# Kernel optimization log

Hardware: AMD Instinct MI355X
Metric: run time of the kernel (lower is better)

## Reference

```python
import jax, jax.numpy as jnp
import numpy as np
from jax import lax

M_RANGE = 1  # padding = m_range, kernel is (2*m_range+1)^2 = 9 classes of 3x3


def _conv(x, kernel):
    # torch F.conv2d (cross-correlation), stride 1, padding M_RANGE
    return lax.conv_general_dilated(
        x, kernel, window_strides=(1, 1),
        padding=[(M_RANGE, M_RANGE), (M_RANGE, M_RANGE)],
        dimension_numbers=('NCHW', 'OIHW', 'NCHW'))


def _construct_seg(ones, m_mask, m_kernel):
    # ones.expand_as(m_mask) * m_mask, then per-sample conv2d -> batched conv
    return _conv(ones * m_mask, m_kernel)  # [B,1,H,W]


def _construct_image(im, m_mask, appear, m_kernel):
    # im: [B,C,H,W]; m_mask: [B,K,H,W]; appear: [B,1,H,W]
    im = im * appear
    B, C, H, W = im.shape
    K = m_mask.shape[1]
    # fuse the python double loop: fold (B,C) into batch, conv K->1 once
    im_expand = (im[:, :, None, :, :] * m_mask[:, None, :, :, :]).reshape(B * C, K, H, W)
    return _conv(im_expand, m_kernel).reshape(B, C, H, W)


def setup_inputs() -> dict:
    key = jax.random.key(0)
    k0, k1, k2, k3 = jax.random.split(key, 4)
    B, C, H, W, K, N_INPUTS = 32, 3, 256, 256, 9, 2
    im_input_f = jax.random.uniform(k0, (B, N_INPUTS * C, H, W), dtype=jnp.float32)
    im_input_b = jax.random.uniform(k1, (B, N_INPUTS * C, H, W), dtype=jnp.float32)
    ones = jnp.ones((B, 1, H, W), dtype=jnp.float32)
    # gt motion masks: soft per-pixel distribution over K motion classes
    gt_motion_f = jax.nn.softmax(jax.random.normal(k2, (B, K, H, W), dtype=jnp.float32), axis=1)
    gt_motion_b = jax.nn.softmax(jax.random.normal(k3, (B, K, H, W), dtype=jnp.float32), axis=1)
    # one-hot displacement kernels: kernel i has a 1 at flat position i of the 3x3 window
    m_kernel = jnp.eye(K, dtype=jnp.float32).reshape(K, 3, 3)[None]  # [1,K,3,3]
    return {"im_input_f": im_input_f, "im_input_b": im_input_b, "ones": ones,
            "gt_motion_f": gt_motion_f, "gt_motion_b": gt_motion_b, "m_kernel": m_kernel}


def reference(im_input_f, im_input_b, ones, gt_motion_f, gt_motion_b, m_kernel):
    IM_CHANNEL = 3
    relu = jax.nn.relu
    m_mask_f, m_mask_b = gt_motion_f, gt_motion_b

    seg_f = _construct_seg(ones, m_mask_f, m_kernel)
    seg_b = _construct_seg(ones, m_mask_b, m_kernel)

    disappear_f = relu(seg_f - 1)
    appear_f = relu(1 - disappear_f)
    disappear_b = relu(seg_b - 1)
    appear_b = relu(1 - disappear_b)

    pred_f = _construct_image(im_input_f[:, -IM_CHANNEL:, :, :], m_mask_f, appear_f, m_kernel)
    pred_b = _construct_image(im_input_b[:, -IM_CHANNEL:, :, :], m_mask_b, appear_b, m_kernel)

    seg_f = 1 - relu(1 - seg_f)
    seg_b = 1 - relu(1 - seg_b)
    attn = (seg_f + 1e-5) / (seg_f + seg_b + 2e-5)  # [B,1,H,W], broadcasts over C
    pred = attn * pred_f + (1 - attn) * pred_b
    return (pred, m_mask_f, 1 - appear_f, attn, m_mask_b, 1 - appear_b, 1 - attn)
```

## Files before the change

kernel.cpp:

```cpp
#include <hip/hip_runtime.h>

#define BB 32
#define KK 9
#define CC 3
#define HH 256
#define WW 256
#define HW (HH * WW)

#define SZ_P ((size_t)BB * CC * HW)
#define SZ_M ((size_t)BB * KK * HW)
#define SZ_S ((size_t)BB * HW)

#define TX 64
#define TY 16
#define TILES_X (WW / TX)
#define TILES_Y (HH / TY)
#define TILES_PER_B (TILES_X * TILES_Y)

__global__ __launch_bounds__(256) void fused_binet_kernel(
    const float* __restrict__ im_f, const float* __restrict__ im_b,
    const float* __restrict__ gt_f, const float* __restrict__ gt_b,
    float* __restrict__ out) {
  __shared__ float s_sf[TY + 2][TX + 2];
  __shared__ float s_sb[TY + 2][TX + 2];

  int bid = blockIdx.x;
  int b = bid / TILES_PER_B;
  int t = bid % TILES_PER_B;
  int ty0 = (t / TILES_X) * TY;
  int tx0 = (t % TILES_X) * TX;

  const float* gf  = gt_f + (size_t)b * KK * HW;
  const float* gb  = gt_b + (size_t)b * KK * HW;
  const float* imf = im_f + ((size_t)b * 6 + 3) * HW;
  const float* imb = im_b + ((size_t)b * 6 + 3) * HW;

  int tid = threadIdx.x;

  for (int i = tid; i < (TY + 2) * (TX + 2); i += 256) {
    int ly = i / (TX + 2);
    int lx = i - ly * (TX + 2);
    int y = ty0 + ly - 1;
    int x = tx0 + lx - 1;
    float sf = 0.f, sb = 0.f;
    if (y >= 0 && y < HH && x >= 0 && x < WW) {
#pragma unroll
      for (int k = 0; k < KK; ++k) {
        int yy = y + (k / 3) - 1;
        int xx = x + (k % 3) - 1;
        if (yy >= 0 && yy < HH && xx >= 0 && xx < WW) {
          int off = k * HW + (yy << 8) + xx;
          sf += gf[off];
          sb += gb[off];
        }
      }
    }
    s_sf[ly][lx] = sf;
    s_sb[ly][lx] = sb;
  }
  __syncthreads();

  float* o_mf     = out + SZ_P;
  float* o_disf   = out + SZ_P + SZ_M;
  float* o_attn   = o_disf + SZ_S;
  float* o_mb     = o_attn + SZ_S;
  float* o_disb   = o_mb + SZ_M;
  float* o_1mattn = o_disb + SZ_S;

  int lx  = tid & (TX - 1);
  int ly0 = tid >> 6;

#pragma unroll
  for (int r = 0; r < 4; ++r) {
    int ly = ly0 + r * 4;
    int h = ty0 + ly;
    int w = tx0 + lx;
    int hw = (h << 8) + w;
    size_t sidx = (size_t)b * HW + hw;

    float sf = s_sf[ly + 1][lx + 1];
    float sb = s_sb[ly + 1][lx + 1];
    float dis_f = fmaxf(sf - 1.f, 0.f);
    float app_f = fmaxf(1.f - dis_f, 0.f);
    float dis_b = fmaxf(sb - 1.f, 0.f);
    float app_b = fmaxf(1.f - dis_b, 0.f);
    float sfc = 1.f - fmaxf(1.f - sf, 0.f);
    float sbc = 1.f - fmaxf(1.f - sb, 0.f);
    float attn = (sfc + 1e-5f) / (sfc + sbc + 2e-5f);

    o_disf[sidx]   = 1.f - app_f;
    o_attn[sidx]   = attn;
    o_disb[sidx]   = 1.f - app_b;
    o_1mattn[sidx] = 1.f - attn;

    float pf0 = 0.f, pf1 = 0.f, pf2 = 0.f;
    float pb0 = 0.f, pb1 = 0.f, pb2 = 0.f;
#pragma unroll
    for (int k = 0; k < KK; ++k) {
      size_t moff = (size_t)b * KK * HW + (size_t)k * HW + hw;
      o_mf[moff] = gf[k * HW + hw];
      o_mb[moff] = gb[k * HW + hw];

      int y = h + (k / 3) - 1;
      int x = w + (k % 3) - 1;
      if (y >= 0 && y < HH && x >= 0 && x < WW) {
        int p = (y << 8) + x;
        float sfq = s_sf[ly + (k / 3)][lx + (k % 3)];
        float af = fmaxf(1.f - fmaxf(sfq - 1.f, 0.f), 0.f);
        float cf = af * gf[k * HW + p];
        pf0 = fmaf(cf, imf[p], pf0);
        pf1 = fmaf(cf, imf[HW + p], pf1);
        pf2 = fmaf(cf, imf[2 * HW + p], pf2);
        float sbq = s_sb[ly + (k / 3)][lx + (k % 3)];
        float ab = fmaxf(1.f - fmaxf(sbq - 1.f, 0.f), 0.f);
        float cb = ab * gb[k * HW + p];
        pb0 = fmaf(cb, imb[p], pb0);
        pb1 = fmaf(cb, imb[HW + p], pb1);
        pb2 = fmaf(cb, imb[2 * HW + p], pb2);
      }
    }
    float at2 = 1.f - attn;
    size_t pbase = (size_t)b * CC * HW + hw;
    out[pbase]          = fmaf(attn, pf0, at2 * pb0);
    out[pbase + HW]     = fmaf(attn, pf1, at2 * pb1);
    out[pbase + 2 * HW] = fmaf(attn, pf2, at2 * pb2);
  }
}

extern "C" void kernel_launch(void* const* d_in, const int* in_sizes, int n_in,
                              void* d_out, int out_size, void* d_ws, size_t ws_size,
                              hipStream_t stream) {
  const float* im_f = (const float*)d_in[0];
  const float* im_b = (const float*)d_in[1];
  const float* gt_f = (const float*)d_in[3];
  const float* gt_b = (const float*)d_in[4];
  float* out = (float*)d_out;

  dim3 block(256);
  dim3 grid(BB * TILES_PER_B);

  fused_binet_kernel<<<grid, block, 0, stream>>>(im_f, im_b, gt_f, gt_b, out);
}
```

Before: 458.0 us.

## Rewrite fused kernel with full-row tiles, float4 vectors, shuffles and nontemporal stores

Each block now covers full 256-wide rows, 8 rows per block, with one wavefront per row and each lane owning 4 consecutive pixels. Horizontal neighbours come from wavefront shuffles instead of redundant global reads. The forward and backward passes run one after the other through a shared 10-row seg buffer. Mask copies and outputs use float4 nontemporal stores, and block IDs are swizzled. This is meant to cut the redundant scalar global loads of the old tiled version and raise memory efficiency, at the cost of higher register pressure from holding nine float4 mask rows per pass.

```diff
diff --git a/kernel.cpp b/kernel.cpp
--- a/kernel.cpp
+++ b/kernel.cpp
@@ -11,120 +11,171 @@
 #define SZ_M ((size_t)BB * KK * HW)
 #define SZ_S ((size_t)BB * HW)
 
-#define TX 64
-#define TY 16
-#define TILES_X (WW / TX)
-#define TILES_Y (HH / TY)
-#define TILES_PER_B (TILES_X * TILES_Y)
+typedef float f4 __attribute__((ext_vector_type(4)));
 
-__global__ __launch_bounds__(256) void fused_binet_kernel(
+__device__ __forceinline__ f4 ld4(const float* p) { return *(const f4*)p; }
+__device__ __forceinline__ void ntst4(float* p, f4 v) {
+  __builtin_nontemporal_store(v, (f4*)p);
+}
+__device__ __forceinline__ f4 vmax4(f4 a, f4 b) {
+  return __builtin_elementwise_max(a, b);
+}
+__device__ __forceinline__ f4 app4(f4 s) {
+  f4 one = {1.f, 1.f, 1.f, 1.f}, z = {0.f, 0.f, 0.f, 0.f};
+  return vmax4(one - vmax4(s - one, z), z);
+}
+__device__ __forceinline__ float app1(float s) {
+  return fmaxf(1.f - fmaxf(s - 1.f, 0.f), 0.f);
+}
+__device__ __forceinline__ f4 shiftwin(f4 v, int dx, int lane) {
+  if (dx == 0) {
+    float l = __shfl_up(v.w, 1);
+    if (lane == 0) l = 0.f;
+    return (f4){l, v.x, v.y, v.z};
+  } else if (dx == 2) {
+    float r = __shfl_down(v.x, 1);
+    if (lane == 63) r = 0.f;
+    return (f4){v.y, v.z, v.w, r};
+  }
+  return v;
+}
+
+__device__ __forceinline__ void run_pass(
+    const float* __restrict__ g,
+    const float* __restrict__ im,
+    float* __restrict__ o_m,
+    float (*s_seg)[WW],
+    int w, int lane, int x0, int y0, int y, size_t hw,
+    f4& seg_out, f4& p0, f4& p1, f4& p2) {
+  const f4 z = {0.f, 0.f, 0.f, 0.f};
+  f4 r[KK];
+  f4 seg = z;
+#pragma unroll
+  for (int k = 0; k < KK; ++k) {
+    const int dy = k / 3, dx = k % 3;
+    int yr = y + dy - 1;
+    f4 v = z;
+    if ((unsigned)yr < HH)
+      v = ld4(g + (size_t)k * HW + ((size_t)yr << 8) + x0);
+    f4 wv = shiftwin(v, dx, lane);
+    r[k] = wv;
+    seg += wv;
+    f4 c = (dy == 1) ? v : ld4(g + (size_t)k * HW + hw);
+    ntst4(o_m + (size_t)k * HW + hw, c);
+  }
+  *(f4*)&s_seg[w + 1][x0] = seg;
+
+  if (w < 2) {
+    int lr = (w == 0) ? 0 : 9;
+    int yh = (w == 0) ? y0 - 1 : y0 + 8;
+    f4 s = z;
+#pragma unroll
+    for (int k = 0; k < KK; ++k) {
+      const int dy = k / 3, dx = k % 3;
+      int yr = yh + dy - 1;
+      f4 v = z;
+      if ((unsigned)yr < HH)
+        v = ld4(g + (size_t)k * HW + ((size_t)yr << 8) + x0);
+      s += shiftwin(v, dx, lane);
+    }
+    *(f4*)&s_seg[lr][x0] = s;
+  }
+  __syncthreads();
+
+  p0 = z; p1 = z; p2 = z;
+#pragma unroll
+  for (int dy = 0; dy < 3; ++dy) {
+    const float* srow = s_seg[w + dy];
+    f4 sc = *(const f4*)&srow[x0];
+    float sl = srow[(x0 == 0) ? 0 : (x0 - 1)];
+    float sr = srow[(x0 == WW - 4) ? (WW - 1) : (x0 + 4)];
+    f4 ac = app4(sc);
+    float al = app1(sl), ar = app1(sr);
+
+    int yr = y + dy - 1;
+    f4 i0 = z, i1 = z, i2 = z;
+    if ((unsigned)yr < HH) {
+      size_t rb = ((size_t)yr << 8) + x0;
+      i0 = ld4(im + rb);
+      i1 = ld4(im + HW + rb);
+      i2 = ld4(im + 2 * HW + rb);
+    }
+    float i0l = __shfl_up(i0.w, 1), i0r = __shfl_down(i0.x, 1);
+    float i1l = __shfl_up(i1.w, 1), i1r = __shfl_down(i1.x, 1);
+    float i2l = __shfl_up(i2.w, 1), i2r = __shfl_down(i2.x, 1);
+#pragma unroll
+    for (int dx = 0; dx < 3; ++dx) {
+      const int k = 3 * dy + dx;
+      f4 aw = (dx == 0) ? (f4){al, ac.x, ac.y, ac.z}
+            : (dx == 2) ? (f4){ac.y, ac.z, ac.w, ar} : ac;
+      f4 c = aw * r[k];
+      f4 w0 = (dx == 0) ? (f4){i0l, i0.x, i0.y, i0.z}
+            : (dx == 2) ? (f4){i0.y, i0.z, i0.w, i0r} : i0;
+      f4 w1 = (dx == 0) ? (f4){i1l, i1.x, i1.y, i1.z}
+            : (dx == 2) ? (f4){i1.y, i1.z, i1.w, i1r} : i1;
+      f4 w2 = (dx == 0) ? (f4){i2l, i2.x, i2.y, i2.z}
+            : (dx == 2) ? (f4){i2.y, i2.z, i2.w, i2r} : i2;
+      p0 += c * w0;
+      p1 += c * w1;
+      p2 += c * w2;
+    }
+  }
+  __syncthreads();
+  seg_out = seg;
+}
+
+__global__ __launch_bounds__(512) void fused_binet_kernel(
     const float* __restrict__ im_f, const float* __restrict__ im_b,
     const float* __restrict__ gt_f, const float* __restrict__ gt_b,
     float* __restrict__ out) {
-  __shared__ float s_sf[TY + 2][TX + 2];
-  __shared__ float s_sb[TY + 2][TX + 2];
+  __shared__ float s_seg[10][WW];
 
   int bid = blockIdx.x;
-  int b = bid / TILES_PER_B;
-  int t = bid % TILES_PER_B;
-  int ty0 = (t / TILES_X) * TY;
-  int tx0 = (t % TILES_X) * TX;
+  int actual = ((bid & 7) << 7) | (bid >> 3);
+  int b  = actual >> 5;
+  int y0 = (actual & 31) << 3;
+
+  int tid  = threadIdx.x;
+  int w    = tid >> 6;
+  int lane = tid & 63;
+  int x0   = lane << 2;
+  int y    = y0 + w;
+  size_t hw = ((size_t)y << 8) + x0;
 
   const float* gf  = gt_f + (size_t)b * KK * HW;
   const float* gb  = gt_b + (size_t)b * KK * HW;
   const float* imf = im_f + ((size_t)b * 6 + 3) * HW;
   const float* imb = im_b + ((size_t)b * 6 + 3) * HW;
 
-  int tid = threadIdx.x;
-
-  for (int i = tid; i < (TY + 2) * (TX + 2); i += 256) {
-    int ly = i / (TX + 2);
-    int lx = i - ly * (TX + 2);
-    int y = ty0 + ly - 1;
-    int x = tx0 + lx - 1;
-    float sf = 0.f, sb = 0.f;
-    if (y >= 0 && y < HH && x >= 0 && x < WW) {
-#pragma unroll
-      for (int k = 0; k < KK; ++k) {
-        int yy = y + (k / 3) - 1;
-        int xx = x + (k % 3) - 1;
-        if (yy >= 0 && yy < HH && xx >= 0 && xx < WW) {
-          int off = k * HW + (yy << 8) + xx;
-          sf += gf[off];
-          sb += gb[off];
-        }
-      }
-    }
-    s_sf[ly][lx] = sf;
-    s_sb[ly][lx] = sb;
-  }
-  __syncthreads();
-
-  float* o_mf     = out + SZ_P;
+  float* o_mf     = out + SZ_P + (size_t)b * KK * HW;
   float* o_disf   = out + SZ_P + SZ_M;
   float* o_attn   = o_disf + SZ_S;
-  float* o_mb     = o_attn + SZ_S;
-  float* o_disb   = o_mb + SZ_M;
+  float* o_mb     = o_attn + SZ_S + (size_t)b * KK * HW;
+  float* o_disb   = o_attn + SZ_S + SZ_M;
   float* o_1mattn = o_disb + SZ_S;
 
-  int lx  = tid & (TX - 1);
-  int ly0 = tid >> 6;
+  f4 segf, segb, pf0, pf1, pf2, pb0, pb1, pb2;
+  run_pass(gf, imf, o_mf, s_seg, w, lane, x0, y0, y, hw, segf, pf0, pf1, pf2);
+  run_pass(gb, imb, o_mb, s_seg, w, lane, x0, y0, y, hw, segb, pb0, pb1, pb2);
 
-#pragma unroll
-  for (int r = 0; r < 4; ++r) {
-    int ly = ly0 + r * 4;
-    int h = ty0 + ly;
-    int w = tx0 + lx;
-    int hw = (h << 8) + w;
-    size_t sidx = (size_t)b * HW + hw;
+  f4 one = {1.f, 1.f, 1.f, 1.f}, z = {0.f, 0.f, 0.f, 0.f};
+  f4 appf = app4(segf);
+  f4 appb = app4(segb);
+  f4 sfc = one - vmax4(one - segf, z);
+  f4 sbc = one - vmax4(one - segb, z);
+  f4 attn = (sfc + 1e-5f) / (sfc + sbc + 2e-5f);
+  f4 at2 = one - attn;
 
-    float sf = s_sf[ly + 1][lx + 1];
-    float sb = s_sb[ly + 1][lx + 1];
-    float dis_f = fmaxf(sf - 1.f, 0.f);
-    float app_f = fmaxf(1.f - dis_f, 0.f);
-    float dis_b = fmaxf(sb - 1.f, 0.f);
-    float app_b = fmaxf(1.f - dis_b, 0.f);
-    float sfc = 1.f - fmaxf(1.f - sf, 0.f);
-    float sbc = 1.f - fmaxf(1.f - sb, 0.f);
-    float attn = (sfc + 1e-5f) / (sfc + sbc + 2e-5f);
+  size_t sidx = (size_t)b * HW + hw;
+  ntst4(o_disf + sidx, one - appf);
+  ntst4(o_attn + sidx, attn);
+  ntst4(o_disb + sidx, one - appb);
+  ntst4(o_1mattn + sidx, one - attn);
 
-    o_disf[sidx]   = 1.f - app_f;
-    o_attn[sidx]   = attn;
-    o_disb[sidx]   = 1.f - app_b;
-    o_1mattn[sidx] = 1.f - attn;
-
-    float pf0 = 0.f, pf1 = 0.f, pf2 = 0.f;
-    float pb0 = 0.f, pb1 = 0.f, pb2 = 0.f;
-#pragma unroll
-    for (int k = 0; k < KK; ++k) {
-      size_t moff = (size_t)b * KK * HW + (size_t)k * HW + hw;
-      o_mf[moff] = gf[k * HW + hw];
-      o_mb[moff] = gb[k * HW + hw];
-
-      int y = h + (k / 3) - 1;
-      int x = w + (k % 3) - 1;
-      if (y >= 0 && y < HH && x >= 0 && x < WW) {
-        int p = (y << 8) + x;
-        float sfq = s_sf[ly + (k / 3)][lx + (k % 3)];
-        float af = fmaxf(1.f - fmaxf(sfq - 1.f, 0.f), 0.f);
-        float cf = af * gf[k * HW + p];
-        pf0 = fmaf(cf, imf[p], pf0);
-        pf1 = fmaf(cf, imf[HW + p], pf1);
-        pf2 = fmaf(cf, imf[2 * HW + p], pf2);
-        float sbq = s_sb[ly + (k / 3)][lx + (k % 3)];
-        float ab = fmaxf(1.f - fmaxf(sbq - 1.f, 0.f), 0.f);
-        float cb = ab * gb[k * HW + p];
-        pb0 = fmaf(cb, imb[p], pb0);
-        pb1 = fmaf(cb, imb[HW + p], pb1);
-        pb2 = fmaf(cb, imb[2 * HW + p], pb2);
-      }
-    }
-    float at2 = 1.f - attn;
-    size_t pbase = (size_t)b * CC * HW + hw;
-    out[pbase]          = fmaf(attn, pf0, at2 * pb0);
-    out[pbase + HW]     = fmaf(attn, pf1, at2 * pb1);
-    out[pbase + 2 * HW] = fmaf(attn, pf2, at2 * pb2);
-  }
+  size_t pbase = (size_t)b * CC * HW + hw;
+  ntst4(out + pbase,          attn * pf0 + at2 * pb0);
+  ntst4(out + pbase + HW,     attn * pf1 + at2 * pb1);
+  ntst4(out + pbase + 2 * HW, attn * pf2 + at2 * pb2);
 }
 
 extern "C" void kernel_launch(void* const* d_in, const int* in_sizes, int n_in,
@@ -136,8 +187,8 @@
   const float* gt_b = (const float*)d_in[4];
   float* out = (float*)d_out;
 
-  dim3 block(256);
-  dim3 grid(BB * TILES_PER_B);
+  dim3 block(512);
+  dim3 grid(BB * 32);
 
   fused_binet_kernel<<<grid, block, 0, stream>>>(im_f, im_b, gt_f, gt_b, out);
 }
```

Measured after the change: 391.0 us. 14.6% less time.
